# Performance work log

Measured on AMD Instinct MI355X. Metric: run time of the kernel, lower is better.

## Reference

```python
import jax, jax.numpy as jnp
import numpy as np

B, T, DIM = 2, 2048, 2048
N_HEAD, N_GROUP = 16, 4
KV_HEAD = N_HEAD // N_GROUP
HEAD_DIM = DIM // N_HEAD


def setup_inputs() -> dict:
    key = jax.random.key(0)
    ks = jax.random.split(key, 7)
    x = jax.random.normal(ks[0], (B, T, DIM), dtype=jnp.float32)
    # rotary tables: last dim = head_dim // 2 (interleaved real/imag pairs)
    pos = jnp.arange(T, dtype=jnp.float32)[:, None]
    inv_freq = 1.0 / (10000.0 ** (jnp.arange(0, HEAD_DIM, 2, dtype=jnp.float32) / HEAD_DIM))
    angles = pos * inv_freq[None, :]  # [T, HEAD_DIM//2]
    freqs_cos = jnp.cos(angles)
    freqs_sin = jnp.sin(angles)
    scale = 0.02
    wq = jax.random.normal(ks[1], (DIM, N_HEAD * HEAD_DIM), dtype=jnp.float32) * scale
    wk = jax.random.normal(ks[2], (DIM, KV_HEAD * HEAD_DIM), dtype=jnp.float32) * scale
    wv = jax.random.normal(ks[3], (DIM, KV_HEAD * HEAD_DIM), dtype=jnp.float32) * scale
    wo = jax.random.normal(ks[4], (N_HEAD * HEAD_DIM, DIM), dtype=jnp.float32) * scale
    return {"x": x, "freqs_cos": freqs_cos, "freqs_sin": freqs_sin,
            "wq": wq, "wk": wk, "wv": wv, "wo": wo}


def _apply_rope(t, cos, sin):
    # t: [B, T, H, D]; interleaved pairs (..., -1, 2) as in torch reference
    tr = t.reshape(*t.shape[:-1], -1, 2)
    r, i = tr[..., 0], tr[..., 1]
    c = cos[None, :, None, :]  # [1, T, 1, D//2]
    s = sin[None, :, None, :]
    out = jnp.stack([r * c - i * s, r * s + i * c], axis=-1)
    return out.reshape(t.shape)


def reference(x, freqs_cos, freqs_sin, wq, wk, wv, wo):
    Bx, Tx, C = x.shape
    xq = (x @ wq).reshape(Bx, Tx, N_HEAD, HEAD_DIM)
    xk = (x @ wk).reshape(Bx, Tx, KV_HEAD, HEAD_DIM)
    xv = (x @ wv).reshape(Bx, Tx, KV_HEAD, HEAD_DIM)
    xq = _apply_rope(xq, freqs_cos, freqs_sin)
    xk = _apply_rope(xk, freqs_cos, freqs_sin)
    # repeat_kv: each kv head repeated n_group times consecutively
    xk = jnp.repeat(xk, N_GROUP, axis=2)  # [B, T, N_HEAD, D]
    xv = jnp.repeat(xv, N_GROUP, axis=2)
    scale = HEAD_DIM ** -0.5
    att = jnp.einsum('bqhd,bkhd->bhqk', xq, xk) * scale
    causal = jnp.tril(jnp.ones((Tx, Tx), dtype=bool))
    att = jnp.where(causal[None, None], att, -jnp.inf)
    att = jax.nn.softmax(att, axis=-1)
    out = jnp.einsum('bhqk,bkhd->bqhd', att, xv).reshape(Bx, Tx, N_HEAD * HEAD_DIM)
    return out @ wo
```

## Files before the change

kernel.cpp:

```cpp
#include <hip/hip_runtime.h>

#define TB 2
#define TT 2048
#define TDIM 2048
#define NHEADS 16
#define KVHEADS 4
#define HD 128

typedef unsigned short u16;
typedef unsigned int u32;
typedef __attribute__((ext_vector_type(8))) short short8;
typedef __attribute__((ext_vector_type(4))) float float4_t;

__device__ __forceinline__ float b2f(u16 u) {
    union { u32 i; float f; } v; v.i = ((u32)u) << 16; return v.f;
}
__device__ __forceinline__ u16 f2b(float f) {
    union { float f; u32 i; } v; v.f = f;
    u32 r = (v.i + 0x7FFFu + ((v.i >> 16) & 1u)) >> 16;
    return (u16)r;
}
__device__ __forceinline__ u32 fbits(float f) {
    union { float f; u32 i; } v; v.f = f; return v.i;
}

__device__ __forceinline__ void gl_lds16(const void* g, void* l) {
    __builtin_amdgcn_global_load_lds((const __attribute__((address_space(1))) void*)g,
                                     (__attribute__((address_space(3))) void*)l, 16, 0, 0);
}

template <bool F32OUT, bool ROPE>
__global__ __launch_bounds__(256, 3)
void gemm_bt(const u16* __restrict__ A, const u16* __restrict__ BT,
             void* __restrict__ Cv, int M, int N, int K,
             const float* __restrict__ fc, const float* __restrict__ fs) {
    __shared__ __align__(16) u16 As[128 * 64];
    __shared__ __align__(16) u16 Bs[128 * 64];
    const int tid  = threadIdx.x;
    const int wave = tid >> 6, lane = tid & 63;
    const int quad = lane >> 4, l16 = lane & 15;
    const int wm = wave >> 1, wn = wave & 1;
    const int row0 = blockIdx.y * 128, col0 = blockIdx.x * 128;

    float4_t acc[4][4];
#pragma unroll
    for (int i = 0; i < 4; i++)
#pragma unroll
        for (int j = 0; j < 4; j++) acc[i][j] = (float4_t){0.f, 0.f, 0.f, 0.f};

    for (int kk = 0; kk < K; kk += 64) {
        __syncthreads();
#pragma unroll
        for (int i = 0; i < 4; i++) {
            int n = i * 256 + wave * 64 + lane;
            int r = n >> 3, c = (n & 7) ^ (r & 7);
            gl_lds16(A  + (size_t)(row0 + r) * K + kk + c * 8, &As[(i * 256 + wave * 64) * 8]);
            gl_lds16(BT + (size_t)(col0 + r) * K + kk + c * 8, &Bs[(i * 256 + wave * 64) * 8]);
        }
        __syncthreads();
#pragma unroll
        for (int ks = 0; ks < 2; ks++) {
            short8 af[4], bf[4];
#pragma unroll
            for (int mt = 0; mt < 4; mt++) {
                int m = wm * 64 + mt * 16 + l16;
                af[mt] = *(const short8*)&As[(m * 8 + ((ks * 4 + quad) ^ (l16 & 7))) * 8];
            }
#pragma unroll
            for (int nt = 0; nt < 4; nt++) {
                int n = wn * 64 + nt * 16 + l16;
                bf[nt] = *(const short8*)&Bs[(n * 8 + ((ks * 4 + quad) ^ (l16 & 7))) * 8];
            }
#pragma unroll
            for (int mt = 0; mt < 4; mt++)
#pragma unroll
                for (int nt = 0; nt < 4; nt++)
                    acc[mt][nt] = __builtin_amdgcn_mfma_f32_16x16x32_bf16(
                        af[mt], bf[nt], acc[mt][nt], 0, 0, 0);
        }
    }
    const bool do_rope = ROPE && (col0 < 2560);
#pragma unroll
    for (int mt = 0; mt < 4; mt++)
#pragma unroll
        for (int nt = 0; nt < 4; nt++)
#pragma unroll
            for (int r = 0; r < 4; r++) {
                int row = row0 + wm * 64 + mt * 16 + quad * 4 + r;
                int col = col0 + wn * 64 + nt * 16 + l16;
                float v = acc[mt][nt][r];
                if (ROPE && do_rope) {
                    float other = __shfl_xor(v, 1, 64);
                    int t = row & (TT - 1);
                    int i0 = (col & (HD - 1)) >> 1;
                    float c = fc[t * 64 + i0], s = fs[t * 64 + i0];
                    v = (col & 1) ? fmaf(v, c, other * s) : fmaf(v, c, -other * s);
                }
                if (F32OUT)
                    ((float*)Cv)[(size_t)row * N + col] = v;
                else
                    ((u16*)Cv)[(size_t)row * N + col] = f2b(v);
            }
}

__global__ void cvt_transpose4(const float* __restrict__ wq, const float* __restrict__ wk,
                               const float* __restrict__ wv, const float* __restrict__ wo,
                               u16* __restrict__ WT, u16* __restrict__ woT) {
    int bx = blockIdx.x;
    const float* in; u16* out; int cols, cx;
    if (bx < 64)      { in = wq; out = WT;                         cols = 2048; cx = bx; }
    else if (bx < 80) { in = wk; out = WT + (size_t)2048 * 2048;   cols = 512;  cx = bx - 64; }
    else if (bx < 96) { in = wv; out = WT + (size_t)2560 * 2048;   cols = 512;  cx = bx - 80; }
    else              { in = wo; out = woT;                        cols = 2048; cx = bx - 96; }
    const int rows = 2048;
    __shared__ u16 tile[32][33];
    int c0 = cx * 32, r0 = blockIdx.y * 32;
    int tx = threadIdx.x & 31, ty = threadIdx.x >> 5;
#pragma unroll
    for (int i = 0; i < 4; i++)
        tile[ty + i * 8][tx] = f2b(in[(size_t)(r0 + ty + i * 8) * cols + c0 + tx]);
    __syncthreads();
#pragma unroll
    for (int i = 0; i < 4; i++)
        out[(size_t)(c0 + ty + i * 8) * rows + r0 + tx] = tile[tx][ty + i * 8];
}

__global__ void cvt_bf16(const float* __restrict__ in, u16* __restrict__ out) {
    size_t i = ((size_t)blockIdx.x * 256 + threadIdx.x) * 4;
    float4 v = *(const float4*)(in + i);
    ushort4 o;
    o.x = f2b(v.x); o.y = f2b(v.y); o.z = f2b(v.z); o.w = f2b(v.w);
    *(ushort4*)(out + i) = o;
}

__global__ void transpose_v(const u16* __restrict__ QKV, u16* __restrict__ Vt) {
    int z = blockIdx.z, b = z >> 2, kv = z & 3;
    const u16* in = QKV + (size_t)b * TT * 3072 + 2560 + kv * HD;
    u16* out = Vt + (size_t)z * HD * TT;
    __shared__ u16 tile[32][33];
    int t0 = blockIdx.x * 32, d0 = blockIdx.y * 32;
    int tx = threadIdx.x & 31, ty = threadIdx.x >> 5;
#pragma unroll
    for (int i = 0; i < 4; i++)
        tile[ty + i * 8][tx] = in[(size_t)(t0 + ty + i * 8) * 3072 + d0 + tx];
    __syncthreads();
#pragma unroll
    for (int i = 0; i < 4; i++)
        out[(size_t)(d0 + ty + i * 8) * TT + t0 + tx] = tile[tx][ty + i * 8];
}

#define PSTR 72
__global__ __launch_bounds__(256, 2)
void attn(const u16* __restrict__ QKV, const u16* __restrict__ Vt,
          u16* __restrict__ O) {
    const int x  = blockIdx.x;
    const int y  = blockIdx.y;
    const int b  = y >> 3;
    const int hp = y & 7;
    const int kvh = hp >> 1;
    const int hb  = kvh * 4 + (hp & 1) * 2;
    const int qb  = b ? (31 - x) : x;
    const int tid = threadIdx.x, w = tid >> 6, lane = tid & 63;
    const int quad = lane >> 4, l16 = lane & 15;

    __shared__ __align__(16) u16 Ks[2][64 * 128];
    __shared__ __align__(16) u16 Vs[128 * 64];
    __shared__ __align__(16) u16 Ps[8][16 * PSTR];

    const u16* Kbase = QKV + (size_t)b * TT * 3072 + 2048 + kvh * HD;
    const u16* Vbase = Vt + (size_t)(b * 4 + kvh) * HD * TT;
    const float Cl = 0.12753102474f;

    auto stageK = [&](int kt, int bb) {
#pragma unroll
        for (int i = 0; i < 4; i++) {
            int n = i * 256 + w * 64 + lane;
            int r = n >> 4, c = (n & 15) ^ (r & 15);
            gl_lds16(Kbase + (size_t)(kt * 64 + r) * 3072 + c * 8,
                     &Ks[bb][(i * 256 + w * 64) * 8]);
        }
    };
    auto stageV = [&](int kt) {
#pragma unroll
        for (int i = 0; i < 4; i++) {
            int n = i * 256 + w * 64 + lane;
            int d = n >> 3, c = (n & 7) ^ (d & 7);
            gl_lds16(Vbase + (size_t)d * TT + kt * 64 + c * 8,
                     &Vs[(i * 256 + w * 64) * 8]);
        }
    };

    stageK(0, 0);

    short8 qf[2][4];
#pragma unroll
    for (int hd = 0; hd < 2; hd++) {
        const u16* Qrow = QKV + ((size_t)b * TT + qb * 64 + w * 16 + l16) * 3072
                          + (hb + hd) * HD;
#pragma unroll
        for (int ks = 0; ks < 4; ks++)
            qf[hd][ks] = *(const short8*)(Qrow + ks * 32 + quad * 8);
    }

    float4_t o[2][8];
#pragma unroll
    for (int hd = 0; hd < 2; hd++)
#pragma unroll
        for (int i = 0; i < 8; i++) o[hd][i] = (float4_t){0.f, 0.f, 0.f, 0.f};
    float mi[2] = {-1e30f, -1e30f}, li[2] = {0.f, 0.f};
    const int qg = qb * 64 + w * 16 + l16;

    for (int kt = 0; kt <= qb; kt++) {
        const int cur = kt & 1;
        __syncthreads();
        stageV(kt);

        float4_t st[2][4];
#pragma unroll
        for (int hd = 0; hd < 2; hd++)
#pragma unroll
            for (int nt = 0; nt < 4; nt++) st[hd][nt] = (float4_t){0.f, 0.f, 0.f, 0.f};
#pragma unroll
        for (int ks = 0; ks < 4; ks++) {
            short8 af[4];
#pragma unroll
            for (int nt = 0; nt < 4; nt++)
                af[nt] = *(const short8*)&Ks[cur][((nt * 16 + l16) * 16 +
                                                  ((ks * 4 + quad) ^ l16)) * 8];
#pragma unroll
            for (int nt = 0; nt < 4; nt++) {
                st[0][nt] = __builtin_amdgcn_mfma_f32_16x16x32_bf16(
                    af[nt], qf[0][ks], st[0][nt], 0, 0, 0);
                st[1][nt] = __builtin_amdgcn_mfma_f32_16x16x32_bf16(
                    af[nt], qf[1][ks], st[1][nt], 0, 0, 0);
            }
        }

        const bool diag = (kt == qb);
        float alpha[2];
#pragma unroll
        for (int hd = 0; hd < 2; hd++) {
            if (diag) {
#pragma unroll
                for (int nt = 0; nt < 4; nt++)
#pragma unroll
                    for (int r = 0; r < 4; r++) {
                        int key = kt * 64 + nt * 16 + quad * 4 + r;
                        if (key > qg) st[hd][nt][r] = -3e38f;
                    }
            }
            float pm = -3e38f;
#pragma unroll
            for (int nt = 0; nt < 4; nt++)
#pragma unroll
                for (int r = 0; r < 4; r++) pm = fmaxf(pm, st[hd][nt][r]);
            pm = fmaxf(pm, __shfl_xor(pm, 16, 64));
            pm = fmaxf(pm, __shfl_xor(pm, 32, 64));
            float mnew = fmaxf(mi[hd], pm);
            alpha[hd] = __builtin_amdgcn_exp2f((mi[hd] - mnew) * Cl);
            mi[hd] = mnew;
            const float mC = mnew * Cl;
            float rs = 0.f;
#pragma unroll
            for (int nt = 0; nt < 4; nt++)
#pragma unroll
                for (int r = 0; r < 4; r++) {
                    float e = __builtin_amdgcn_exp2f(fmaf(st[hd][nt][r], Cl, -mC));
                    st[hd][nt][r] = e;
                    rs += e;
                }
            rs += __shfl_xor(rs, 16, 64);
            rs += __shfl_xor(rs, 32, 64);
            li[hd] = li[hd] * alpha[hd] + rs;

#pragma unroll
            for (int nt = 0; nt < 4; nt++) {
                uint2 pk;
                pk.x = __builtin_amdgcn_perm(fbits(st[hd][nt][1]), fbits(st[hd][nt][0]), 0x07060302u);
                pk.y = __builtin_amdgcn_perm(fbits(st[hd][nt][3]), fbits(st[hd][nt][2]), 0x07060302u);
                *(uint2*)&Ps[w * 2 + hd][l16 * PSTR + nt * 16 + quad * 4] = pk;
            }
            float a_o[4];
#pragma unroll
            for (int r = 0; r < 4; r++) a_o[r] = __shfl(alpha[hd], quad * 4 + r, 64);
#pragma unroll
            for (int n2 = 0; n2 < 8; n2++)
#pragma unroll
                for (int r = 0; r < 4; r++) o[hd][n2][r] *= a_o[r];
        }

        __syncthreads();
        if (kt < qb) stageK(kt + 1, cur ^ 1);

#pragma unroll
        for (int ks2 = 0; ks2 < 2; ks2++) {
            short8 apA = *(const short8*)&Ps[w * 2 + 0][l16 * PSTR + ks2 * 32 + quad * 8];
            short8 apB = *(const short8*)&Ps[w * 2 + 1][l16 * PSTR + ks2 * 32 + quad * 8];
#pragma unroll
            for (int n2 = 0; n2 < 8; n2++) {
                short8 bv = *(const short8*)&Vs[((n2 * 16 + l16) * 8 +
                                                ((ks2 * 4 + quad) ^ (l16 & 7))) * 8];
                o[0][n2] = __builtin_amdgcn_mfma_f32_16x16x32_bf16(apA, bv, o[0][n2], 0, 0, 0);
                o[1][n2] = __builtin_amdgcn_mfma_f32_16x16x32_bf16(apB, bv, o[1][n2], 0, 0, 0);
            }
        }
    }

#pragma unroll
    for (int hd = 0; hd < 2; hd++) {
        float l_o[4];
#pragma unroll
        for (int r = 0; r < 4; r++) l_o[r] = __shfl(li[hd], quad * 4 + r, 64);
        u16* Ob2 = O + ((size_t)b * TT + qb * 64 + w * 16) * TDIM + (hb + hd) * HD;
#pragma unroll
        for (int n2 = 0; n2 < 8; n2++)
#pragma unroll
            for (int r = 0; r < 4; r++)
                Ob2[(size_t)(quad * 4 + r) * TDIM + n2 * 16 + l16] =
                    f2b(o[hd][n2][r] / l_o[r]);
    }
}

extern "C" void kernel_launch(void* const* d_in, const int* in_sizes, int n_in,
                              void* d_out, int out_size, void* d_ws, size_t ws_size,
                              hipStream_t stream) {
    const float* x  = (const float*)d_in[0];
    const float* fc = (const float*)d_in[1];
    const float* fs = (const float*)d_in[2];
    const float* wq = (const float*)d_in[3];
    const float* wk = (const float*)d_in[4];
    const float* wv = (const float*)d_in[5];
    const float* wo = (const float*)d_in[6];
    float* out = (float*)d_out;

    char* ws = (char*)d_ws;
    size_t off = 0;
    auto alloc = [&](size_t bytes) -> void* {
        void* p = ws + off;
        off += (bytes + 255) & ~(size_t)255;
        return p;
    };
    u16* xb  = (u16*)alloc((size_t)4096 * 2048 * 2);
    u16* WT  = (u16*)alloc((size_t)3072 * 2048 * 2);
    u16* woT = (u16*)alloc((size_t)2048 * 2048 * 2);
    u16* QKV = (u16*)alloc((size_t)4096 * 3072 * 2);
    u16* Vtb = (u16*)alloc((size_t)4096 * 512 * 2);
    u16* Ob  = (u16*)alloc((size_t)4096 * 2048 * 2);

    dim3 blk(256);
    cvt_bf16<<<dim3(8192), blk, 0, stream>>>(x, xb);
    cvt_transpose4<<<dim3(160, 64), blk, 0, stream>>>(wq, wk, wv, wo, WT, woT);
    gemm_bt<false, true><<<dim3(24, 32), blk, 0, stream>>>(
        xb, WT, QKV, 4096, 3072, 2048, fc, fs);
    transpose_v<<<dim3(64, 4, 8), blk, 0, stream>>>(QKV, Vtb);
    attn<<<dim3(32, 16), blk, 0, stream>>>(QKV, Vtb, Ob);
    gemm_bt<true, false><<<dim3(16, 32), blk, 0, stream>>>(
        Ob, woT, out, 4096, 2048, 2048, nullptr, nullptr);
}
```

Before: 288.7 us.

## Use 256x256 eight-wave double-buffered GEMM for the QKV projection

Adds a new GEMM kernel with 512 threads, 256x256 output tiles, and double-buffered LDS staging. The kernel interleaves async global-to-LDS loads of the next K-tiles with MFMA quadrants, using barriers and s_setprio. Only the QKV projection switches to it; the output projection keeps the old kernel. This is meant to raise data reuse per tile and hide load latency. The cost is 128KB of LDS per block and a grid of only 192 blocks, fewer than the 256 CUs, so some CUs sit idle.

```diff
diff --git a/kernel.cpp b/kernel.cpp
--- a/kernel.cpp
+++ b/kernel.cpp
@@ -27,6 +27,156 @@
 __device__ __forceinline__ void gl_lds16(const void* g, void* l) {
     __builtin_amdgcn_global_load_lds((const __attribute__((address_space(1))) void*)g,
                                      (__attribute__((address_space(3))) void*)l, 16, 0, 0);
+}
+
+#define BARF() do { asm volatile("" ::: "memory"); \
+                    __builtin_amdgcn_s_barrier();  \
+                    asm volatile("" ::: "memory"); } while (0)
+
+#define MM16(mh, nh)                                                          \
+    do {                                                                      \
+        __builtin_amdgcn_s_setprio(1);                                        \
+        _Pragma("unroll") for (int ks = 0; ks < 2; ks++)                      \
+        _Pragma("unroll") for (int mq = 0; mq < 4; mq++)                      \
+        _Pragma("unroll") for (int nq = 0; nq < 2; nq++)                      \
+            acc[(mh) * 4 + mq][(nh) * 2 + nq] =                               \
+                __builtin_amdgcn_mfma_f32_16x16x32_bf16(                      \
+                    af[mq][ks], bf[nq][ks],                                   \
+                    acc[(mh) * 4 + mq][(nh) * 2 + nq], 0, 0, 0);              \
+        __builtin_amdgcn_s_setprio(0);                                        \
+    } while (0)
+
+template <bool F32OUT, bool ROPE>
+__global__ __launch_bounds__(512, 2)
+void gemm_bt8(const u16* __restrict__ A, const u16* __restrict__ BT,
+              void* __restrict__ Cv, int M, int N, int K,
+              const float* __restrict__ fc, const float* __restrict__ fs) {
+    __shared__ __align__(16) u16 As[2][256 * 64];
+    __shared__ __align__(16) u16 Bs[2][256 * 64];
+    const int tid  = threadIdx.x;
+    const int w    = tid >> 6, lane = tid & 63;
+    const int quad = lane >> 4, l16 = lane & 15;
+    const int wm = w >> 2, wn = w & 3;
+    const int row0 = blockIdx.y * 256, col0 = blockIdx.x * 256;
+    const int nkt = K >> 6, nit = nkt >> 1;
+
+    float4_t acc[8][4];
+#pragma unroll
+    for (int i = 0; i < 8; i++)
+#pragma unroll
+        for (int j = 0; j < 4; j++) acc[i][j] = (float4_t){0.f, 0.f, 0.f, 0.f};
+
+    auto stA = [&](int half, int T) {
+        if (T >= nkt) return;
+#pragma unroll
+        for (int j = 0; j < 2; j++) {
+            int n = j * 512 + tid;
+            int r = n >> 3, c = (n & 7) ^ (r & 7);
+            gl_lds16(A + (size_t)(row0 + half * 128 + r) * K + T * 64 + c * 8,
+                     &As[T & 1][(half * 1024 + j * 512 + w * 64) * 8]);
+        }
+    };
+    auto stB = [&](int half, int T) {
+        if (T >= nkt) return;
+#pragma unroll
+        for (int j = 0; j < 2; j++) {
+            int n = j * 512 + tid;
+            int r = n >> 3, c = (n & 7) ^ (r & 7);
+            gl_lds16(BT + (size_t)(col0 + half * 128 + r) * K + T * 64 + c * 8,
+                     &Bs[T & 1][(half * 1024 + j * 512 + w * 64) * 8]);
+        }
+    };
+
+    short8 af[4][2], bf[2][2];
+    auto ldA = [&](int mh, int p) {
+#pragma unroll
+        for (int mq = 0; mq < 4; mq++) {
+            int row = mh * 128 + wm * 64 + mq * 16 + l16;
+#pragma unroll
+            for (int ks = 0; ks < 2; ks++)
+                af[mq][ks] = *(const short8*)
+                    &As[p][(row * 8 + ((ks * 4 + quad) ^ (row & 7))) * 8];
+        }
+    };
+    auto ldB = [&](int nh, int p) {
+#pragma unroll
+        for (int nq = 0; nq < 2; nq++) {
+            int row = nh * 128 + wn * 32 + nq * 16 + l16;
+#pragma unroll
+            for (int ks = 0; ks < 2; ks++)
+                bf[nq][ks] = *(const short8*)
+                    &Bs[p][(row * 8 + ((ks * 4 + quad) ^ (row & 7))) * 8];
+        }
+    };
+
+    stA(0, 0); stB(0, 0); stB(1, 0); stA(1, 0);
+    stA(0, 1); stB(1, 1); stA(1, 1);
+    asm volatile("s_waitcnt vmcnt(6)" ::: "memory");
+    __builtin_amdgcn_s_barrier();
+    asm volatile("" ::: "memory");
+
+    for (int i = 0; i < nit; i++) {
+        const int T0 = i * 2;
+        const bool last = (i == nit - 1);
+        ldA(0, 0); ldB(0, 0);
+        stB(0, T0 + 1);
+        BARF(); MM16(0, 0); BARF();
+
+        ldB(1, 0);
+        stA(0, T0 + 2);
+        BARF(); MM16(0, 1); BARF();
+
+        ldA(1, 0);
+        stB(1, T0 + 2);
+        BARF(); MM16(1, 1); BARF();
+
+        ldB(0, 0);
+        stA(1, T0 + 2);
+        if (last) asm volatile("s_waitcnt vmcnt(0)" ::: "memory");
+        else      asm volatile("s_waitcnt vmcnt(6)" ::: "memory");
+        BARF(); MM16(1, 0); BARF();
+
+        ldA(0, 1); ldB(0, 1);
+        stB(0, T0 + 2);
+        BARF(); MM16(0, 0); BARF();
+
+        ldB(1, 1);
+        stA(0, T0 + 3);
+        BARF(); MM16(0, 1); BARF();
+
+        ldA(1, 1);
+        stB(1, T0 + 3);
+        BARF(); MM16(1, 1); BARF();
+
+        ldB(0, 1);
+        stA(1, T0 + 3);
+        if (last) asm volatile("s_waitcnt vmcnt(0)" ::: "memory");
+        else      asm volatile("s_waitcnt vmcnt(6)" ::: "memory");
+        BARF(); MM16(1, 0); BARF();
+    }
+
+    const bool do_rope = ROPE && (col0 < 2560);
+#pragma unroll
+    for (int ai = 0; ai < 8; ai++)
+#pragma unroll
+        for (int bj = 0; bj < 4; bj++)
+#pragma unroll
+            for (int r = 0; r < 4; r++) {
+                int row = row0 + (ai >> 2) * 128 + wm * 64 + (ai & 3) * 16 + quad * 4 + r;
+                int col = col0 + (bj >> 1) * 128 + wn * 32 + (bj & 1) * 16 + l16;
+                float v = acc[ai][bj][r];
+                if (ROPE && do_rope) {
+                    float other = __shfl_xor(v, 1, 64);
+                    int t = row & (TT - 1);
+                    int i0 = (col & (HD - 1)) >> 1;
+                    float c = fc[t * 64 + i0], s = fs[t * 64 + i0];
+                    v = (col & 1) ? fmaf(v, c, other * s) : fmaf(v, c, -other * s);
+                }
+                if (F32OUT)
+                    ((float*)Cv)[(size_t)row * N + col] = v;
+                else
+                    ((u16*)Cv)[(size_t)row * N + col] = f2b(v);
+            }
 }
 
 template <bool F32OUT, bool ROPE>
@@ -350,7 +500,7 @@
     dim3 blk(256);
     cvt_bf16<<<dim3(8192), blk, 0, stream>>>(x, xb);
     cvt_transpose4<<<dim3(160, 64), blk, 0, stream>>>(wq, wk, wv, wo, WT, woT);
-    gemm_bt<false, true><<<dim3(24, 32), blk, 0, stream>>>(
+    gemm_bt8<false, true><<<dim3(12, 16), dim3(512), 0, stream>>>(
         xb, WT, QKV, 4096, 3072, 2048, fc, fs);
     transpose_v<<<dim3(64, 4, 8), blk, 0, stream>>>(QKV, Vtb);
     attn<<<dim3(32, 16), blk, 0, stream>>>(QKV, Vtb, Ob);
```

Measured after the change: 315.4 us. +9.2%, slower.
